# Optimization experiments

Hardware: AMD Instinct MI355X
Metric: run time of the kernel (lower is better)

The kernel has to match this reference:

```python
import jax, jax.numpy as jnp
import numpy as np

T_LEN, E_LEN, BATCH, DIM = 32, 256, 16, 512  # topic_len, exp_len, batch, input=hidden size
HID = 512


def setup_inputs() -> dict:
    key = jax.random.key(0)
    k1, k2, k3, k4, k5, k6 = jax.random.split(key, 6)
    topic = jax.random.normal(k1, (T_LEN, BATCH, DIM), dtype=jnp.float32)
    exp_output = jax.random.normal(k2, (E_LEN, BATCH, DIM), dtype=jnp.float32)
    seq_mask = jax.random.bernoulli(k3, 0.1, (E_LEN, BATCH))  # True = masked exp position
    # nn.Linear(hidden+input, hidden): weight [HID, HID+DIM], bias [HID]
    lim1 = 1.0 / np.sqrt(HID + DIM)
    W_attn = jax.random.uniform(k4, (HID, HID + DIM), minval=-lim1, maxval=lim1, dtype=jnp.float32)
    b_attn = jax.random.uniform(k5, (HID,), minval=-lim1, maxval=lim1, dtype=jnp.float32)
    # nn.Linear(hidden, 1): weight [1, HID], bias [1]
    lim2 = 1.0 / np.sqrt(HID)
    kv, kb = jax.random.split(k6)
    v_score = jax.random.uniform(kv, (1, HID), minval=-lim2, maxval=lim2, dtype=jnp.float32)
    b_score = jax.random.uniform(kb, (1,), minval=-lim2, maxval=lim2, dtype=jnp.float32)
    return {"topic": topic, "exp_output": exp_output, "seq_mask": seq_mask,
            "W_attn": W_attn, "b_attn": b_attn, "v_score": v_score, "b_score": b_score}


def reference(topic, exp_output, seq_mask, W_attn, b_attn, v_score, b_score):
    # topic: [T, B, D]; exp_output: [E, B, D]; seq_mask: [E, B] bool
    D = topic.shape[2]
    # Split the concat-Linear: cat(topic, exp) @ W.T == topic @ W[:, :D].T + exp @ W[:, D:].T
    proj_t = jnp.einsum('tbd,hd->bth', topic, W_attn[:, :D])        # [B, T, H]
    proj_e = jnp.einsum('ebd,hd->beh', exp_output, W_attn[:, D:])   # [B, E, H]
    feat = jnp.tanh(proj_t[:, :, None, :] + proj_e[:, None, :, :] + b_attn)  # [B, T, E, H]
    energies = jnp.einsum('bteh,h->bte', feat, v_score[0]) + b_score[0]      # [B, T, E]
    # mask exp positions (broadcast over topic dim), as masked_fill(-1e12)
    energies = jnp.where(seq_mask.T[:, None, :], jnp.float32(-1e12), energies)
    attn_s1 = jax.nn.softmax(jnp.swapaxes(energies, 1, 2), axis=2)  # [B, E, T], softmax over topics
    attn_s2 = jax.nn.softmax(energies, axis=2)                      # [B, T, E], softmax over exp
    new_exp = jnp.einsum('bet,btd->bed', attn_s1, jnp.swapaxes(topic, 0, 1))       # [B, E, D]
    new_topic = jnp.einsum('bte,bed->btd', attn_s2, jnp.swapaxes(exp_output, 0, 1))  # [B, T, D]
    return new_topic, new_exp
```

## Files before the change

kernel.cpp:

```cpp
#include <hip/hip_runtime.h>
#include <hip/hip_bf16.h>
#include <cstddef>
#include <cstdint>

#define T_LEN 32
#define E_LEN 256
#define BATCH 16
#define DIM 512
#define HID 512
#define WROW 1024

#define TWO_LOG2E 2.8853900817779268f
#define LOG2E 1.4426950408889634f

typedef __attribute__((ext_vector_type(8))) short bf16x8;
typedef __attribute__((ext_vector_type(4))) float f32x4;

__device__ inline bf16x8 cvt8(float4 a, float4 b) {
    union { bf16x8 v; __hip_bfloat16 h[8]; } u;
    u.h[0] = __float2bfloat16(a.x); u.h[1] = __float2bfloat16(a.y);
    u.h[2] = __float2bfloat16(a.z); u.h[3] = __float2bfloat16(a.w);
    u.h[4] = __float2bfloat16(b.x); u.h[5] = __float2bfloat16(b.y);
    u.h[6] = __float2bfloat16(b.z); u.h[7] = __float2bfloat16(b.w);
    return u.v;
}

#define GPAD 8
#define GLDR (64 + GPAD)

__global__ __launch_bounds__(256) void gemm_fused_k(
    const float* __restrict__ topic, const float* __restrict__ expo,
    const float* __restrict__ W, const float* __restrict__ battn,
    float* __restrict__ EPT, __hip_bfloat16* __restrict__ EPE) {
    __shared__ __hip_bfloat16 As[64 * GLDR];
    __shared__ __hip_bfloat16 Bs[64 * GLDR];
    const int tid = threadIdx.x;
    const int by = blockIdx.x >> 3;
    const int n0 = (blockIdx.x & 7) * 64;
    const float* A; const float* Wp; int m0;
    const bool isT = (by < 8);
    if (isT) { A = topic; Wp = W;       m0 = by * 64; }
    else     { A = expo;  Wp = W + DIM; m0 = (by - 8) * 64; }
    const int w = tid >> 6;
    const int lane = tid & 63;
    const int l15 = lane & 15;
    const int g = lane >> 4;
    const int srow = tid >> 2;
    const int sc = tid & 3;

    f32x4 acc[4];
    const f32x4 z = {0.f, 0.f, 0.f, 0.f};
#pragma unroll
    for (int nt = 0; nt < 4; ++nt) acc[nt] = z;

    const float* ga = A + (size_t)(m0 + srow) * 512 + sc * 8;
    const float* gb = Wp + (size_t)(n0 + srow) * WROW + sc * 8;

    float4 a0 = *(const float4*)(ga);
    float4 a1 = *(const float4*)(ga + 4);
    float4 a2 = *(const float4*)(ga + 32);
    float4 a3 = *(const float4*)(ga + 36);
    float4 b0 = *(const float4*)(gb);
    float4 b1 = *(const float4*)(gb + 4);
    float4 b2 = *(const float4*)(gb + 32);
    float4 b3 = *(const float4*)(gb + 36);

    for (int kk = 0; kk < 8; ++kk) {
        bf16x8 av0 = cvt8(a0, a1), av1 = cvt8(a2, a3);
        bf16x8 bv0 = cvt8(b0, b1), bv1 = cvt8(b2, b3);
        if (kk < 7) {
            ga += 64; gb += 64;
            a0 = *(const float4*)(ga);
            a1 = *(const float4*)(ga + 4);
            a2 = *(const float4*)(ga + 32);
            a3 = *(const float4*)(ga + 36);
            b0 = *(const float4*)(gb);
            b1 = *(const float4*)(gb + 4);
            b2 = *(const float4*)(gb + 32);
            b3 = *(const float4*)(gb + 36);
        }
        __syncthreads();
        *(bf16x8*)&As[srow * GLDR + sc * 8] = av0;
        *(bf16x8*)&As[srow * GLDR + sc * 8 + 32] = av1;
        *(bf16x8*)&Bs[srow * GLDR + sc * 8] = bv0;
        *(bf16x8*)&Bs[srow * GLDR + sc * 8 + 32] = bv1;
        __syncthreads();
#pragma unroll
        for (int s = 0; s < 2; ++s) {
            bf16x8 af = *(const bf16x8*)&As[(w * 16 + l15) * GLDR + (s * 4 + g) * 8];
#pragma unroll
            for (int nt = 0; nt < 4; ++nt) {
                bf16x8 bf = *(const bf16x8*)&Bs[(nt * 16 + l15) * GLDR + (s * 4 + g) * 8];
                acc[nt] = __builtin_amdgcn_mfma_f32_16x16x32_bf16(af, bf, acc[nt], 0, 0, 0);
            }
        }
    }
    if (isT) {
#pragma unroll
        for (int nt = 0; nt < 4; ++nt) {
            int n = n0 + nt * 16 + l15;
            float bv = battn[n];
#pragma unroll
            for (int r = 0; r < 4; ++r) {
                int m = m0 + w * 16 + g * 4 + r;
                EPT[(size_t)m * 512 + n] =
                    __builtin_amdgcn_exp2f((acc[nt][r] + bv) * TWO_LOG2E);
            }
        }
    } else {
#pragma unroll
        for (int nt = 0; nt < 4; ++nt) {
            int n = n0 + nt * 16 + l15;
#pragma unroll
            for (int r = 0; r < 4; ++r) {
                int m = m0 + w * 16 + g * 4 + r;
                EPE[(size_t)m * 512 + n] = __float2bfloat16(
                    __builtin_amdgcn_exp2f(acc[nt][r] * TWO_LOG2E));
            }
        }
    }
}

__global__ __launch_bounds__(256) void energies_k(
    const float* __restrict__ EPT, const __hip_bfloat16* __restrict__ EPE,
    const float* __restrict__ v, const int* __restrict__ mask,
    float* __restrict__ P) {
    const int u = blockIdx.x;
    const int b = u & 15;
    const int tg = (u >> 4) & 3;
    const int ech = u >> 6;
    const int tid = threadIdx.x;
    const int lane = tid & 63;
    const int w = tid >> 6;
    const int h0 = lane * 8;
    const int e0 = ech * 16 + w * 4;

    int mk[4];
#pragma unroll
    for (int ei = 0; ei < 4; ++ei) mk[ei] = mask[(e0 + ei) * BATCH + b];

    float sv[8], spt[8][8];
    {
        float4 v0 = *(const float4*)(v + h0);
        float4 v1 = *(const float4*)(v + h0 + 4);
        sv[0] = -2.f * v0.x; sv[1] = -2.f * v0.y; sv[2] = -2.f * v0.z; sv[3] = -2.f * v0.w;
        sv[4] = -2.f * v1.x; sv[5] = -2.f * v1.y; sv[6] = -2.f * v1.z; sv[7] = -2.f * v1.w;
#pragma unroll
        for (int i = 0; i < 8; ++i) {
            const float* p = EPT + ((size_t)((tg * 8 + i) * BATCH + b)) * HID + h0;
            float4 p0 = *(const float4*)(p);
            float4 p1 = *(const float4*)(p + 4);
            spt[i][0] = p0.x; spt[i][1] = p0.y; spt[i][2] = p0.z; spt[i][3] = p0.w;
            spt[i][4] = p1.x; spt[i][5] = p1.y; spt[i][6] = p1.z; spt[i][7] = p1.w;
        }
    }
#pragma unroll
    for (int ei = 0; ei < 4; ++ei) {
        const int e = e0 + ei;
        if (mk[ei] != 0) {
            if (lane < 8)
                P[((size_t)b * T_LEN + tg * 8 + lane) * E_LEN + e] = 1e-30f;
            continue;
        }
        union { bf16x8 v8; __hip_bfloat16 h[8]; } pv;
        pv.v8 = *(const bf16x8*)(EPE + ((size_t)(e * BATCH + b)) * HID + h0);
        float pr[8];
#pragma unroll
        for (int j = 0; j < 8; ++j) pr[j] = __bfloat162float(pv.h[j]);
        float a[8] = {0.f, 0.f, 0.f, 0.f, 0.f, 0.f, 0.f, 0.f};
#pragma unroll
        for (int i = 0; i < 8; ++i) {
#pragma unroll
            for (int j = 0; j < 8; ++j) {
                float q = fmaf(spt[i][j], pr[j], 1.0f);
                float r = __builtin_amdgcn_rcpf(q);
                a[i] = fmaf(sv[j], r, a[i]);
            }
        }
#pragma unroll
        for (int i = 0; i < 8; ++i) {
            a[i] += __shfl_xor(a[i], 1);
            a[i] += __shfl_xor(a[i], 2);
            a[i] += __shfl_xor(a[i], 4);
            a[i] += __shfl_xor(a[i], 8);
        }
        const int sel = lane & 3;
        float uA = sel == 0 ? a[0] : sel == 1 ? a[1] : sel == 2 ? a[2] : a[3];
        float uB = sel == 0 ? a[4] : sel == 1 ? a[5] : sel == 2 ? a[6] : a[7];
        uA += __shfl_xor(uA, 16); uA += __shfl_xor(uA, 32);
        uB += __shfl_xor(uB, 16); uB += __shfl_xor(uB, 32);
        float uu = (lane & 4) ? uB : uA;
        if (lane < 8)
            P[((size_t)b * T_LEN + tg * 8 + lane) * E_LEN + e] =
                __builtin_amdgcn_exp2f(uu * LOG2E);
    }
}

__global__ __launch_bounds__(256) void epilogue_k(
    const float* __restrict__ P, const float* __restrict__ topic,
    const float* __restrict__ expo, float* __restrict__ out) {
    __shared__ float smem[5120];
    const int tid = threadIdx.x;
    const int lane = tid & 63;
    const int w = tid >> 6;
    if (blockIdx.x < 512) {
        const int b = blockIdx.x >> 5;
        const int ech = (blockIdx.x >> 1) & 15;
        const int hf = blockIdx.x & 1;
        const int e0 = ech * 16 + w * 4;
        float wv[4];
#pragma unroll
        for (int ei = 0; ei < 4; ++ei) {
            const int e = e0 + ei;
            float x = (lane < T_LEN) ? P[((size_t)b * T_LEN + lane) * E_LEN + e] : 0.f;
            float s = x;
#pragma unroll
            for (int off = 32; off; off >>= 1) s += __shfl_xor(s, off);
            wv[ei] = x * __builtin_amdgcn_rcpf(s);
        }
        const int d0 = hf * 256 + lane * 4;
        float4 acc[4];
#pragma unroll
        for (int ei = 0; ei < 4; ++ei) acc[ei] = {0.f, 0.f, 0.f, 0.f};
        for (int t = 0; t < T_LEN; ++t) {
            float4 r = *(const float4*)(topic + ((size_t)t * BATCH + b) * DIM + d0);
            float wt[4];
#pragma unroll
            for (int ei = 0; ei < 4; ++ei) wt[ei] = __shfl(wv[ei], t);
#pragma unroll
            for (int ei = 0; ei < 4; ++ei) {
                acc[ei].x = fmaf(wt[ei], r.x, acc[ei].x);
                acc[ei].y = fmaf(wt[ei], r.y, acc[ei].y);
                acc[ei].z = fmaf(wt[ei], r.z, acc[ei].z);
                acc[ei].w = fmaf(wt[ei], r.w, acc[ei].w);
            }
        }
#pragma unroll
        for (int ei = 0; ei < 4; ++ei) {
            float* o = out + (size_t)BATCH * T_LEN * DIM +
                       ((size_t)b * E_LEN + e0 + ei) * DIM + d0;
            *(float4*)o = acc[ei];
        }
    } else {
        const int q = blockIdx.x - 512;
        const int b = q >> 4;
        const int tq = (q >> 1) & 7;
        const int hf = q & 1;
        {
            const int bt = b * T_LEN + tq * 4 + w;
            float4 xv = *(const float4*)&P[(size_t)bt * E_LEN + lane * 4];
            float s = xv.x + xv.y + xv.z + xv.w;
#pragma unroll
            for (int off = 32; off; off >>= 1) s += __shfl_xor(s, off);
            float inv = __builtin_amdgcn_rcpf(s);
            float4 wvv = {xv.x * inv, xv.y * inv, xv.z * inv, xv.w * inv};
            *(float4*)&smem[w * 256 + lane * 4] = wvv;
        }
        __syncthreads();
        const int dl = lane * 4;
        const int dglob = hf * 256 + dl;
        float4 a0 = {0.f, 0.f, 0.f, 0.f};
        float4 a1 = {0.f, 0.f, 0.f, 0.f};
        float4 a2 = {0.f, 0.f, 0.f, 0.f};
        float4 a3 = {0.f, 0.f, 0.f, 0.f};
        const float* base = expo + (size_t)b * DIM + dglob;
        for (int ee = 0; ee < 64; ++ee) {
            const int e = w * 64 + ee;
            float4 rv = *(const float4*)(base + (size_t)e * BATCH * DIM);
            float w0 = smem[e];
            float w1 = smem[256 + e];
            float w2 = smem[512 + e];
            float w3 = smem[768 + e];
            a0.x = fmaf(w0, rv.x, a0.x); a0.y = fmaf(w0, rv.y, a0.y);
            a0.z = fmaf(w0, rv.z, a0.z); a0.w = fmaf(w0, rv.w, a0.w);
            a1.x = fmaf(w1, rv.x, a1.x); a1.y = fmaf(w1, rv.y, a1.y);
            a1.z = fmaf(w1, rv.z, a1.z); a1.w = fmaf(w1, rv.w, a1.w);
            a2.x = fmaf(w2, rv.x, a2.x); a2.y = fmaf(w2, rv.y, a2.y);
            a2.z = fmaf(w2, rv.z, a2.z); a2.w = fmaf(w2, rv.w, a2.w);
            a3.x = fmaf(w3, rv.x, a3.x); a3.y = fmaf(w3, rv.y, a3.y);
            a3.z = fmaf(w3, rv.z, a3.z); a3.w = fmaf(w3, rv.w, a3.w);
        }
        *(float4*)&smem[1024 + (w * 4 + 0) * 256 + dl] = a0;
        *(float4*)&smem[1024 + (w * 4 + 1) * 256 + dl] = a1;
        *(float4*)&smem[1024 + (w * 4 + 2) * 256 + dl] = a2;
        *(float4*)&smem[1024 + (w * 4 + 3) * 256 + dl] = a3;
        __syncthreads();
#pragma unroll
        for (int tt = 0; tt < 4; ++tt) {
            float sum = smem[1024 + (0 * 4 + tt) * 256 + tid] +
                        smem[1024 + (1 * 4 + tt) * 256 + tid] +
                        smem[1024 + (2 * 4 + tt) * 256 + tid] +
                        smem[1024 + (3 * 4 + tt) * 256 + tid];
            out[((size_t)b * T_LEN + tq * 4 + tt) * DIM + hf * 256 + tid] = sum;
        }
    }
}

extern "C" void kernel_launch(void* const* d_in, const int* in_sizes, int n_in,
                              void* d_out, int out_size, void* d_ws, size_t ws_size,
                              hipStream_t stream) {
    const float* topic = (const float*)d_in[0];
    const float* expo  = (const float*)d_in[1];
    const int*   mask  = (const int*)d_in[2];
    const float* W     = (const float*)d_in[3];
    const float* battn = (const float*)d_in[4];
    const float* vsc   = (const float*)d_in[5];
    float* out = (float*)d_out;

    float* EPT = (float*)d_ws;
    __hip_bfloat16* EPE = (__hip_bfloat16*)(EPT + 512 * 512);
    float* P = (float*)(EPE + (size_t)4096 * 512);

    gemm_fused_k<<<576, 256, 0, stream>>>(topic, expo, W, battn, EPT, EPE);
    energies_k<<<1024, 256, 0, stream>>>(EPT, EPE, vsc, mask, P);
    epilogue_k<<<768, 256, 0, stream>>>(P, topic, expo, out);
}
```

Before: 113.8 us.

## Fuse three stages into one cooperative kernel and pair reciprocals algebraically

Merges the GEMM, energies and epilogue kernels into a single cooperative-launch persistent kernel of 512 blocks separated by grid-wide syncs, and keeps the three-kernel path as a fallback if the cooperative launch fails. The goal is to remove launch gaps and inter-kernel drain. The energies inner loop also combines terms of the form v/(1+x) in groups of four over a common denominator, so it issues one reciprocal per four terms instead of four. The costs are grid-sync overhead, a 512-block grid whose tail runs unevenly across stages, and possible precision loss or overflow from multiplying denominators together.

```diff
diff --git a/kernel.cpp b/kernel.cpp
--- a/kernel.cpp
+++ b/kernel.cpp
@@ -1,7 +1,10 @@
 #include <hip/hip_runtime.h>
+#include <hip/hip_cooperative_groups.h>
 #include <hip/hip_bf16.h>
 #include <cstddef>
 #include <cstdint>
+
+namespace cg = cooperative_groups;
 
 #define T_LEN 32
 #define E_LEN 256
@@ -28,15 +31,13 @@
 #define GPAD 8
 #define GLDR (64 + GPAD)
 
-__global__ __launch_bounds__(256) void gemm_fused_k(
+__device__ __forceinline__ void gemm_body(
+    int u, int tid, __hip_bfloat16* As, __hip_bfloat16* Bs,
     const float* __restrict__ topic, const float* __restrict__ expo,
     const float* __restrict__ W, const float* __restrict__ battn,
     float* __restrict__ EPT, __hip_bfloat16* __restrict__ EPE) {
-    __shared__ __hip_bfloat16 As[64 * GLDR];
-    __shared__ __hip_bfloat16 Bs[64 * GLDR];
-    const int tid = threadIdx.x;
-    const int by = blockIdx.x >> 3;
-    const int n0 = (blockIdx.x & 7) * 64;
+    const int by = u >> 3;
+    const int n0 = (u & 7) * 64;
     const float* A; const float* Wp; int m0;
     const bool isT = (by < 8);
     if (isT) { A = topic; Wp = W;       m0 = by * 64; }
@@ -121,15 +122,14 @@
     }
 }
 
-__global__ __launch_bounds__(256) void energies_k(
+__device__ __forceinline__ void energies_body(
+    int u, int tid,
     const float* __restrict__ EPT, const __hip_bfloat16* __restrict__ EPE,
     const float* __restrict__ v, const int* __restrict__ mask,
     float* __restrict__ P) {
-    const int u = blockIdx.x;
     const int b = u & 15;
     const int tg = (u >> 4) & 3;
     const int ech = u >> 6;
-    const int tid = threadIdx.x;
     const int lane = tid & 63;
     const int w = tid >> 6;
     const int h0 = lane * 8;
@@ -139,12 +139,14 @@
 #pragma unroll
     for (int ei = 0; ei < 4; ++ei) mk[ei] = mask[(e0 + ei) * BATCH + b];
 
-    float sv[8], spt[8][8];
+    float sv[8], sv2[4], spt[8][8];
     {
         float4 v0 = *(const float4*)(v + h0);
         float4 v1 = *(const float4*)(v + h0 + 4);
         sv[0] = -2.f * v0.x; sv[1] = -2.f * v0.y; sv[2] = -2.f * v0.z; sv[3] = -2.f * v0.w;
         sv[4] = -2.f * v1.x; sv[5] = -2.f * v1.y; sv[6] = -2.f * v1.z; sv[7] = -2.f * v1.w;
+        sv2[0] = sv[0] + sv[1]; sv2[1] = sv[2] + sv[3];
+        sv2[2] = sv[4] + sv[5]; sv2[3] = sv[6] + sv[7];
 #pragma unroll
         for (int i = 0; i < 8; ++i) {
             const float* p = EPT + ((size_t)((tg * 8 + i) * BATCH + b)) * HID + h0;
@@ -171,10 +173,21 @@
 #pragma unroll
         for (int i = 0; i < 8; ++i) {
 #pragma unroll
-            for (int j = 0; j < 8; ++j) {
-                float q = fmaf(spt[i][j], pr[j], 1.0f);
-                float r = __builtin_amdgcn_rcpf(q);
-                a[i] = fmaf(sv[j], r, a[i]);
+            for (int jq = 0; jq < 2; ++jq) {
+                const int j0 = jq * 4;
+                float a0 = spt[i][j0 + 0] * pr[j0 + 0];
+                float a1 = spt[i][j0 + 1] * pr[j0 + 1];
+                float a2 = spt[i][j0 + 2] * pr[j0 + 2];
+                float a3 = spt[i][j0 + 3] * pr[j0 + 3];
+                float u0 = a0 + 1.0f;
+                float u2 = a2 + 1.0f;
+                float d01 = fmaf(a1, u0, u0);
+                float d23 = fmaf(a3, u2, u2);
+                float n01 = fmaf(sv[j0 + 0], a1, fmaf(sv[j0 + 1], a0, sv2[jq * 2 + 0]));
+                float n23 = fmaf(sv[j0 + 2], a3, fmaf(sv[j0 + 3], a2, sv2[jq * 2 + 1]));
+                float nn = fmaf(n01, d23, n23 * d01);
+                float dd = d01 * d23;
+                a[i] = fmaf(nn, __builtin_amdgcn_rcpf(dd), a[i]);
             }
         }
 #pragma unroll
@@ -196,17 +209,16 @@
     }
 }
 
-__global__ __launch_bounds__(256) void epilogue_k(
+__device__ __forceinline__ void epilogue_body(
+    int u, int tid, float* smem,
     const float* __restrict__ P, const float* __restrict__ topic,
     const float* __restrict__ expo, float* __restrict__ out) {
-    __shared__ float smem[5120];
-    const int tid = threadIdx.x;
     const int lane = tid & 63;
     const int w = tid >> 6;
-    if (blockIdx.x < 512) {
-        const int b = blockIdx.x >> 5;
-        const int ech = (blockIdx.x >> 1) & 15;
-        const int hf = blockIdx.x & 1;
+    if (u < 512) {
+        const int b = u >> 5;
+        const int ech = (u >> 1) & 15;
+        const int hf = u & 1;
         const int e0 = ech * 16 + w * 4;
         float wv[4];
 #pragma unroll
@@ -242,7 +254,7 @@
             *(float4*)o = acc[ei];
         }
     } else {
-        const int q = blockIdx.x - 512;
+        const int q = u - 512;
         const int b = q >> 4;
         const int tq = (q >> 1) & 7;
         const int hf = q & 1;
@@ -293,7 +305,55 @@
                         smem[1024 + (3 * 4 + tt) * 256 + tid];
             out[((size_t)b * T_LEN + tq * 4 + tt) * DIM + hf * 256 + tid] = sum;
         }
-    }
+        __syncthreads();
+    }
+}
+
+__global__ __launch_bounds__(256, 2) void fused_k(
+    const float* __restrict__ topic, const float* __restrict__ expo,
+    const float* __restrict__ W, const float* __restrict__ battn,
+    const float* __restrict__ vsc, const int* __restrict__ mask,
+    float* __restrict__ EPT, __hip_bfloat16* __restrict__ EPE,
+    float* __restrict__ P, float* __restrict__ out) {
+    __shared__ __align__(16) float smem[5120];
+    const int tid = threadIdx.x;
+    const int bid = blockIdx.x;
+    cg::grid_group grid = cg::this_grid();
+    {
+        __hip_bfloat16* As = (__hip_bfloat16*)smem;
+        __hip_bfloat16* Bs = As + 64 * GLDR;
+        for (int u = bid; u < 576; u += 512)
+            gemm_body(u, tid, As, Bs, topic, expo, W, battn, EPT, EPE);
+    }
+    grid.sync();
+    for (int u = bid; u < 1024; u += 512)
+        energies_body(u, tid, EPT, EPE, vsc, mask, P);
+    grid.sync();
+    for (int u = bid; u < 768; u += 512)
+        epilogue_body(u, tid, smem, P, topic, expo, out);
+}
+
+__global__ __launch_bounds__(256) void gemm_fused_k(
+    const float* __restrict__ topic, const float* __restrict__ expo,
+    const float* __restrict__ W, const float* __restrict__ battn,
+    float* __restrict__ EPT, __hip_bfloat16* __restrict__ EPE) {
+    __shared__ __align__(16) __hip_bfloat16 As[64 * GLDR];
+    __shared__ __align__(16) __hip_bfloat16 Bs[64 * GLDR];
+    gemm_body(blockIdx.x, threadIdx.x, As, Bs, topic, expo, W, battn, EPT, EPE);
+}
+
+__global__ __launch_bounds__(256) void energies_k(
+    const float* __restrict__ EPT, const __hip_bfloat16* __restrict__ EPE,
+    const float* __restrict__ v, const int* __restrict__ mask,
+    float* __restrict__ P) {
+    energies_body(blockIdx.x, threadIdx.x, EPT, EPE, v, mask, P);
+}
+
+__global__ __launch_bounds__(256) void epilogue_k(
+    const float* __restrict__ P, const float* __restrict__ topic,
+    const float* __restrict__ expo, float* __restrict__ out) {
+    __shared__ __align__(16) float smem[5120];
+    epilogue_body(blockIdx.x, threadIdx.x, smem, P, topic, expo, out);
 }
 
 extern "C" void kernel_launch(void* const* d_in, const int* in_sizes, int n_in,
@@ -311,7 +371,15 @@
     __hip_bfloat16* EPE = (__hip_bfloat16*)(EPT + 512 * 512);
     float* P = (float*)(EPE + (size_t)4096 * 512);
 
-    gemm_fused_k<<<576, 256, 0, stream>>>(topic, expo, W, battn, EPT, EPE);
-    energies_k<<<1024, 256, 0, stream>>>(EPT, EPE, vsc, mask, P);
-    epilogue_k<<<768, 256, 0, stream>>>(P, topic, expo, out);
-}
+    void* args[10] = {(void*)&topic, (void*)&expo, (void*)&W, (void*)&battn,
+                      (void*)&vsc, (void*)&mask, (void*)&EPT, (void*)&EPE,
+                      (void*)&P, (void*)&out};
+    hipError_t err = hipLaunchCooperativeKernel((const void*)fused_k,
+                                                dim3(512), dim3(256),
+                                                args, 0, stream);
+    if (err != hipSuccess) {
+        gemm_fused_k<<<576, 256, 0, stream>>>(topic, expo, W, battn, EPT, EPE);
+        energies_k<<<1024, 256, 0, stream>>>(EPT, EPE, vsc, mask, P);
+        epilogue_k<<<768, 256, 0, stream>>>(P, topic, expo, out);
+    }
+}
```

After: 251.4 us. 121% more time.

## Combine four reciprocals into one in energies and double-buffer GEMM LDS tiles

Applied to the files above, without the earlier changes.

The energies inner loop now adds four terms of the form sv/(1+x) over a common denominator, so it needs one rcp per four hidden elements instead of one per element. This cuts transcendental-unit pressure in the hot loop at the cost of extra FMAs and a larger risk of overflow or precision loss in the product of the denominators. Separately, the GEMM kernel double-buffers its shared-memory A/B tiles, which removes one __syncthreads per K step.

```diff
diff --git a/kernel.cpp b/kernel.cpp
--- a/kernel.cpp
+++ b/kernel.cpp
@@ -32,8 +32,8 @@
     const float* __restrict__ topic, const float* __restrict__ expo,
     const float* __restrict__ W, const float* __restrict__ battn,
     float* __restrict__ EPT, __hip_bfloat16* __restrict__ EPE) {
-    __shared__ __hip_bfloat16 As[64 * GLDR];
-    __shared__ __hip_bfloat16 Bs[64 * GLDR];
+    __shared__ __align__(16) __hip_bfloat16 As[2][64 * GLDR];
+    __shared__ __align__(16) __hip_bfloat16 Bs[2][64 * GLDR];
     const int tid = threadIdx.x;
     const int by = blockIdx.x >> 3;
     const int n0 = (blockIdx.x & 7) * 64;
@@ -66,6 +66,7 @@
     float4 b3 = *(const float4*)(gb + 36);
 
     for (int kk = 0; kk < 8; ++kk) {
+        const int cur = kk & 1;
         bf16x8 av0 = cvt8(a0, a1), av1 = cvt8(a2, a3);
         bf16x8 bv0 = cvt8(b0, b1), bv1 = cvt8(b2, b3);
         if (kk < 7) {
@@ -79,18 +80,17 @@
             b2 = *(const float4*)(gb + 32);
             b3 = *(const float4*)(gb + 36);
         }
+        *(bf16x8*)&As[cur][srow * GLDR + sc * 8] = av0;
+        *(bf16x8*)&As[cur][srow * GLDR + sc * 8 + 32] = av1;
+        *(bf16x8*)&Bs[cur][srow * GLDR + sc * 8] = bv0;
+        *(bf16x8*)&Bs[cur][srow * GLDR + sc * 8 + 32] = bv1;
         __syncthreads();
-        *(bf16x8*)&As[srow * GLDR + sc * 8] = av0;
-        *(bf16x8*)&As[srow * GLDR + sc * 8 + 32] = av1;
-        *(bf16x8*)&Bs[srow * GLDR + sc * 8] = bv0;
-        *(bf16x8*)&Bs[srow * GLDR + sc * 8 + 32] = bv1;
-        __syncthreads();
 #pragma unroll
         for (int s = 0; s < 2; ++s) {
-            bf16x8 af = *(const bf16x8*)&As[(w * 16 + l15) * GLDR + (s * 4 + g) * 8];
+            bf16x8 af = *(const bf16x8*)&As[cur][(w * 16 + l15) * GLDR + (s * 4 + g) * 8];
 #pragma unroll
             for (int nt = 0; nt < 4; ++nt) {
-                bf16x8 bf = *(const bf16x8*)&Bs[(nt * 16 + l15) * GLDR + (s * 4 + g) * 8];
+                bf16x8 bf = *(const bf16x8*)&Bs[cur][(nt * 16 + l15) * GLDR + (s * 4 + g) * 8];
                 acc[nt] = __builtin_amdgcn_mfma_f32_16x16x32_bf16(af, bf, acc[nt], 0, 0, 0);
             }
         }
@@ -139,12 +139,14 @@
 #pragma unroll
     for (int ei = 0; ei < 4; ++ei) mk[ei] = mask[(e0 + ei) * BATCH + b];
 
-    float sv[8], spt[8][8];
+    float sv[8], sv2[4], spt[8][8];
     {
         float4 v0 = *(const float4*)(v + h0);
         float4 v1 = *(const float4*)(v + h0 + 4);
         sv[0] = -2.f * v0.x; sv[1] = -2.f * v0.y; sv[2] = -2.f * v0.z; sv[3] = -2.f * v0.w;
         sv[4] = -2.f * v1.x; sv[5] = -2.f * v1.y; sv[6] = -2.f * v1.z; sv[7] = -2.f * v1.w;
+        sv2[0] = sv[0] + sv[1]; sv2[1] = sv[2] + sv[3];
+        sv2[2] = sv[4] + sv[5]; sv2[3] = sv[6] + sv[7];
 #pragma unroll
         for (int i = 0; i < 8; ++i) {
             const float* p = EPT + ((size_t)((tg * 8 + i) * BATCH + b)) * HID + h0;
@@ -171,10 +173,21 @@
 #pragma unroll
         for (int i = 0; i < 8; ++i) {
 #pragma unroll
-            for (int j = 0; j < 8; ++j) {
-                float q = fmaf(spt[i][j], pr[j], 1.0f);
-                float r = __builtin_amdgcn_rcpf(q);
-                a[i] = fmaf(sv[j], r, a[i]);
+            for (int jq = 0; jq < 2; ++jq) {
+                const int j0 = jq * 4;
+                float a0 = spt[i][j0 + 0] * pr[j0 + 0];
+                float a1 = spt[i][j0 + 1] * pr[j0 + 1];
+                float a2 = spt[i][j0 + 2] * pr[j0 + 2];
+                float a3 = spt[i][j0 + 3] * pr[j0 + 3];
+                float u0 = a0 + 1.0f;
+                float u2 = a2 + 1.0f;
+                float d01 = fmaf(a1, u0, u0);
+                float d23 = fmaf(a3, u2, u2);
+                float n01 = fmaf(sv[j0 + 0], a1, fmaf(sv[j0 + 1], a0, sv2[jq * 2 + 0]));
+                float n23 = fmaf(sv[j0 + 2], a3, fmaf(sv[j0 + 3], a2, sv2[jq * 2 + 1]));
+                float nn = fmaf(n01, d23, n23 * d01);
+                float dd = d01 * d23;
+                a[i] = fmaf(nn, __builtin_amdgcn_rcpf(dd), a[i]);
             }
         }
 #pragma unroll
@@ -199,7 +212,7 @@
 __global__ __launch_bounds__(256) void epilogue_k(
     const float* __restrict__ P, const float* __restrict__ topic,
     const float* __restrict__ expo, float* __restrict__ out) {
-    __shared__ float smem[5120];
+    __shared__ __align__(16) float smem[5120];
     const int tid = threadIdx.x;
     const int lane = tid & 63;
     const int w = tid >> 6;
```

New measurement: 113.6 us. Within noise of the previous version (-0.1%).
